# Optimization experiments

Hardware: AMD Instinct MI355X
Metric: run time of the kernel (lower is better)

Reference implementation:

```python
import jax, jax.numpy as jnp
import numpy as np

V, D, J = 1024, 1024, 1024  # num_outputs, predictor_dim, joiner_dim
B, U = 64, 512
NULL_INDEX = 0


def setup_inputs() -> dict:
    key = jax.random.key(0)
    ks = jax.random.split(key, 9)
    s = 0.02
    return {
        "y": jax.random.randint(ks[0], (B, U), 0, V, dtype=jnp.int64) if jax.config.jax_enable_x64 else jax.random.randint(ks[0], (B, U), 0, V, dtype=jnp.int32),
        "embed": jax.random.normal(ks[1], (V, D), jnp.float32) * s,
        "weight_ih": jax.random.normal(ks[2], (3 * D, D), jnp.float32) * s,
        "bias_ih": jax.random.normal(ks[3], (3 * D,), jnp.float32) * s,
        "weight_hh": jax.random.normal(ks[4], (3 * D, D), jnp.float32) * s,
        "bias_hh": jax.random.normal(ks[5], (3 * D,), jnp.float32) * s,
        "linear_w": jax.random.normal(ks[6], (J, D), jnp.float32) * s,
        "linear_b": jax.random.normal(ks[7], (J,), jnp.float32) * s,
        "initial_state": jax.random.normal(ks[8], (D,), jnp.float32),
    }


def reference(y, embed, weight_ih, bias_ih, weight_hh, bias_hh, linear_w, linear_b, initial_state):
    b, u_len = y.shape
    d = initial_state.shape[0]
    # Decoder input sequence: start symbol (NULL_INDEX=0) then the labels -> length U+1
    tokens = jnp.concatenate([jnp.full((b, 1), NULL_INDEX, dtype=y.dtype), y], axis=1)  # [B, U+1]
    x = embed[tokens]  # [B, U+1, D]
    # Precompute input-side gate pre-activations for all steps (batched GEMM)
    gx = jnp.einsum("bud,gd->bug", x, weight_ih) + bias_ih  # [B, U+1, 3D]
    h0 = jnp.broadcast_to(initial_state, (b, d))

    def step(h, gx_t):
        # PyTorch GRUCell: gates ordered (r, z, n)
        gh = h @ weight_hh.T + bias_hh  # [B, 3D]
        r = jax.nn.sigmoid(gx_t[:, :d] + gh[:, :d])
        z = jax.nn.sigmoid(gx_t[:, d:2 * d] + gh[:, d:2 * d])
        n = jnp.tanh(gx_t[:, 2 * d:] + r * gh[:, 2 * d:])
        h_new = (1.0 - z) * n + z * h
        return h_new, h_new

    _, hs = jax.lax.scan(step, h0, jnp.swapaxes(gx, 0, 1))  # hs: [U+1, B, D]
    out = jnp.einsum("ubd,jd->buj", hs, linear_w) + linear_b  # [B, U+1, J]
    return out
```

## Files before the change

### kernel.cpp

```cpp
#include <hip/hip_runtime.h>
#include <hip/hip_bf16.h>

typedef float f32x4 __attribute__((ext_vector_type(4)));
typedef short s16x8 __attribute__((ext_vector_type(8)));
typedef int   i32x4 __attribute__((ext_vector_type(4)));
typedef _Float16 h16x8 __attribute__((ext_vector_type(8)));

#define NV 1024
#define ND 1024
#define NJ 1024
#define NB 64
#define NU 512
#define NT 513
#define G3 3072
#define SLOT 65536
#define NWG 64

static __device__ __forceinline__ unsigned short f2h(float f) {
  union { _Float16 h; unsigned short u; } x; x.h = (_Float16)f;
  return x.u;
}

static __device__ __forceinline__ void unswizzle(long e, int& r, int& k) {
  long blk = e >> 9; int l = (int)((e >> 3) & 63); int j = (int)(e & 7);
  r = (int)(blk >> 5) * 16 + (l & 15);
  k = ((int)(blk & 31)) * 32 + ((l >> 4) << 3) + j;
}

__global__ void predictor_prep(const float* __restrict__ whh, const float* __restrict__ wih,
                               const float* __restrict__ em, const float* __restrict__ lw,
                               const float* __restrict__ bih, const float* __restrict__ bhh,
                               const float* __restrict__ init,
                               unsigned short* __restrict__ wh_sw, unsigned short* __restrict__ wi_sw,
                               unsigned short* __restrict__ em_sw, unsigned short* __restrict__ lw_sw,
                               float* __restrict__ bias_sum, unsigned short* __restrict__ hs,
                               unsigned int* __restrict__ flags) {
  long e = (long)blockIdx.x * 256 + threadIdx.x;
  const long nbig = 3145728, nsm = 1048576;
  if (e < nbig) { int r, k; unswizzle(e, r, k); wh_sw[e] = f2h(whh[(long)r * 1024 + k]); return; }
  e -= nbig;
  if (e < nbig) { int r, k; unswizzle(e, r, k); wi_sw[e] = f2h(wih[(long)r * 1024 + k]); return; }
  e -= nbig;
  if (e < nsm) { int r, k; unswizzle(e, r, k); em_sw[e] = f2h(em[(long)r * 1024 + k]); return; }
  e -= nsm;
  if (e < nsm) { int r, k; unswizzle(e, r, k); lw_sw[e] = f2h(lw[(long)r * 1024 + k]); return; }
  e -= nsm;
  if (e < 65536) { int r, k; unswizzle(e, r, k); hs[e] = f2h(init[k]); return; }
  e -= 65536;
  if (e < 3072) { bias_sum[e] = bih[e] + bhh[e]; return; }
  e -= 3072;
  if (e < 128) flags[e] = 0u;
}

__global__ __launch_bounds__(256) void predictor_gemm(
    const unsigned short* __restrict__ A, long a_chunk_stride,
    const unsigned short* __restrict__ Bw,
    const float* __restrict__ bias, float* __restrict__ out,
    int rowmul_i, int rowmul_c, int out_stride) {
  const int nt = blockIdx.x, chunk = blockIdx.y;
  const int tid = threadIdx.x, lane = tid & 63, wave = tid >> 6;
  const unsigned short* Ab = A + (long)chunk * a_chunk_stride + wave * 16384 + lane * 8;
  const unsigned short* Bb = Bw + (long)nt * 65536 + lane * 8;
  f32x4 a0 = {0,0,0,0}, a1 = {0,0,0,0}, a2 = {0,0,0,0}, a3 = {0,0,0,0};
#pragma unroll 4
  for (int kc = 0; kc < 32; ++kc) {
    h16x8 av = __builtin_bit_cast(h16x8, *(const s16x8*)(Ab + kc * 512));
    h16x8 w0 = __builtin_bit_cast(h16x8, *(const s16x8*)(Bb + kc * 512));
    h16x8 w1 = __builtin_bit_cast(h16x8, *(const s16x8*)(Bb + 16384 + kc * 512));
    h16x8 w2 = __builtin_bit_cast(h16x8, *(const s16x8*)(Bb + 32768 + kc * 512));
    h16x8 w3 = __builtin_bit_cast(h16x8, *(const s16x8*)(Bb + 49152 + kc * 512));
    a0 = __builtin_amdgcn_mfma_f32_16x16x32_f16(av, w0, a0, 0, 0, 0);
    a1 = __builtin_amdgcn_mfma_f32_16x16x32_f16(av, w1, a1, 0, 0, 0);
    a2 = __builtin_amdgcn_mfma_f32_16x16x32_f16(av, w2, a2, 0, 0, 0);
    a3 = __builtin_amdgcn_mfma_f32_16x16x32_f16(av, w3, a3, 0, 0, 0);
  }
  const int q = lane >> 4, nl = lane & 15, colbase = nt << 6;
#pragma unroll
  for (int j = 0; j < 4; ++j) {
    int il = (wave << 4) + (q << 2) + j;
    long row = (long)il * rowmul_i + (long)chunk * rowmul_c;
    float* orow = out + row * out_stride + colbase;
    orow[nl]      = a0[j] + bias[colbase + nl];
    orow[16 + nl] = a1[j] + bias[colbase + 16 + nl];
    orow[32 + nl] = a2[j] + bias[colbase + 32 + nl];
    orow[48 + nl] = a3[j] + bias[colbase + 48 + nl];
  }
}

#define PINSTAGE(CNT, B)                                                        \
  asm volatile("s_waitcnt vmcnt(" #CNT ")"                                      \
    : "+v"(hf[(B)*8+0]), "+v"(hf[(B)*8+1]), "+v"(hf[(B)*8+2]), "+v"(hf[(B)*8+3]), \
      "+v"(hf[(B)*8+4]), "+v"(hf[(B)*8+5]), "+v"(hf[(B)*8+6]), "+v"(hf[(B)*8+7]) :: "memory")

__global__ __launch_bounds__(256, 1) void predictor_rnn(
    const unsigned short* __restrict__ wh_sw, const float* __restrict__ gtab,
    const int* __restrict__ y, const float* __restrict__ init,
    unsigned short* __restrict__ hs, unsigned short* __restrict__ flags) {
  __shared__ float buf[4][3][4][64][4];
  __shared__ unsigned short tbuf[1024];
  const int wg = blockIdx.x, tid = threadIdx.x, lane = tid & 63, w = tid >> 6;
  const int q = lane >> 4, dloc = lane & 15, dg = (wg << 4) + dloc;

  h16x8 wrf[8], wzf[8], wnf[8];
#pragma unroll
  for (int i = 0; i < 8; ++i) {
    int kc = (w << 3) + i;
    wrf[i] = __builtin_bit_cast(h16x8, *(const s16x8*)(wh_sw + ((long)(      wg) << 14) + kc * 512 + lane * 8));
    wzf[i] = __builtin_bit_cast(h16x8, *(const s16x8*)(wh_sw + ((long)( 64 + wg) << 14) + kc * 512 + lane * 8));
    wnf[i] = __builtin_bit_cast(h16x8, *(const s16x8*)(wh_sw + ((long)(128 + wg) << 14) + kc * 512 + lane * 8));
  }
  float hreg[4];
#pragma unroll
  for (int j = 0; j < 4; ++j) hreg[j] = init[dg];

  const unsigned short* fpoll = flags + (w << 6) + lane;
  unsigned short* fpub = flags + ((wg >> 4) << 6) + ((wg & 15) << 2) + w;

  for (int t = 1; t <= NT; ++t) {
    float gr[4], gz[4], gn[4];
#pragma unroll
    for (int j = 0; j < 4; ++j) {
      int b = (w << 4) + (q << 2) + j;
      int tok = (t == 1) ? 0 : y[b * NU + (t - 2)];
      const float* g = gtab + (long)tok * G3 + dg;
      asm volatile("global_load_dword %0, %1, off" : "=v"(gr[j]) : "v"(g) : "memory");
      asm volatile("global_load_dword %0, %1, off" : "=v"(gz[j]) : "v"(g + 1024) : "memory");
      asm volatile("global_load_dword %0, %1, off" : "=v"(gn[j]) : "v"(g + 2048) : "memory");
    }

    if (t > 1) {
      const unsigned int tm1 = (unsigned)(t - 1);
      for (;;) {
        unsigned int v;
        asm volatile("global_load_ushort %0, %1, off sc1" : "=v"(v) : "v"(fpoll) : "memory");
        asm volatile("s_waitcnt vmcnt(0)" : "+v"(v) :: "memory");
        if (__all((int)(v >= tm1))) break;
        __builtin_amdgcn_s_sleep(1);
      }
    }
    asm volatile("s_waitcnt vmcnt(0)"
      : "+v"(gr[0]), "+v"(gr[1]), "+v"(gr[2]), "+v"(gr[3]),
        "+v"(gz[0]), "+v"(gz[1]), "+v"(gz[2]), "+v"(gz[3]),
        "+v"(gn[0]), "+v"(gn[1]), "+v"(gn[2]), "+v"(gn[3]) :: "memory");

    const unsigned short* hprev = hs + (long)(t - 1) * SLOT;
    unsigned short* hcur = hs + (long)t * SLOT;

    i32x4 hf[32];
#pragma unroll
    for (int bg = 0; bg < 4; ++bg)
#pragma unroll
      for (int i = 0; i < 8; ++i) {
        const unsigned short* a = hprev + bg * 16384 + ((w << 3) + i) * 512 + lane * 8;
        asm volatile("global_load_dwordx4 %0, %1, off sc1" : "=v"(hf[bg * 8 + i]) : "v"(a) : "memory");
      }
    f32x4 aR[4], aZ[4], aN[4];
#pragma unroll
    for (int bg = 0; bg < 4; ++bg) { aR[bg] = (f32x4){0,0,0,0}; aZ[bg] = (f32x4){0,0,0,0}; aN[bg] = (f32x4){0,0,0,0}; }
    {
      PINSTAGE(24, 0);
#pragma unroll
      for (int i = 0; i < 8; ++i) { h16x8 a = __builtin_bit_cast(h16x8, hf[0 * 8 + i]);
        aR[0] = __builtin_amdgcn_mfma_f32_16x16x32_f16(a, wrf[i], aR[0], 0, 0, 0);
        aZ[0] = __builtin_amdgcn_mfma_f32_16x16x32_f16(a, wzf[i], aZ[0], 0, 0, 0);
        aN[0] = __builtin_amdgcn_mfma_f32_16x16x32_f16(a, wnf[i], aN[0], 0, 0, 0); }
      PINSTAGE(16, 1);
#pragma unroll
      for (int i = 0; i < 8; ++i) { h16x8 a = __builtin_bit_cast(h16x8, hf[1 * 8 + i]);
        aR[1] = __builtin_amdgcn_mfma_f32_16x16x32_f16(a, wrf[i], aR[1], 0, 0, 0);
        aZ[1] = __builtin_amdgcn_mfma_f32_16x16x32_f16(a, wzf[i], aZ[1], 0, 0, 0);
        aN[1] = __builtin_amdgcn_mfma_f32_16x16x32_f16(a, wnf[i], aN[1], 0, 0, 0); }
      PINSTAGE(8, 2);
#pragma unroll
      for (int i = 0; i < 8; ++i) { h16x8 a = __builtin_bit_cast(h16x8, hf[2 * 8 + i]);
        aR[2] = __builtin_amdgcn_mfma_f32_16x16x32_f16(a, wrf[i], aR[2], 0, 0, 0);
        aZ[2] = __builtin_amdgcn_mfma_f32_16x16x32_f16(a, wzf[i], aZ[2], 0, 0, 0);
        aN[2] = __builtin_amdgcn_mfma_f32_16x16x32_f16(a, wnf[i], aN[2], 0, 0, 0); }
      PINSTAGE(0, 3);
#pragma unroll
      for (int i = 0; i < 8; ++i) { h16x8 a = __builtin_bit_cast(h16x8, hf[3 * 8 + i]);
        aR[3] = __builtin_amdgcn_mfma_f32_16x16x32_f16(a, wrf[i], aR[3], 0, 0, 0);
        aZ[3] = __builtin_amdgcn_mfma_f32_16x16x32_f16(a, wzf[i], aZ[3], 0, 0, 0);
        aN[3] = __builtin_amdgcn_mfma_f32_16x16x32_f16(a, wnf[i], aN[3], 0, 0, 0); }
    }

#pragma unroll
    for (int b2 = 0; b2 < 4; ++b2)
      if (b2 != w) {
        *(f32x4*)&buf[w][0][b2][lane][0] = aR[b2];
        *(f32x4*)&buf[w][1][b2][lane][0] = aZ[b2];
        *(f32x4*)&buf[w][2][b2][lane][0] = aN[b2];
      }
    __syncthreads();
    f32x4 sR = aR[w], sZ = aZ[w], sN = aN[w];
#pragma unroll
    for (int v = 0; v < 4; ++v)
      if (v != w) {
        sR += *(const f32x4*)&buf[v][0][w][lane][0];
        sZ += *(const f32x4*)&buf[v][1][w][lane][0];
        sN += *(const f32x4*)&buf[v][2][w][lane][0];
      }
    __syncthreads();

#pragma unroll
    for (int j = 0; j < 4; ++j) {
      float r = 1.f / (1.f + __expf(-(gr[j] + sR[j])));
      float z = 1.f / (1.f + __expf(-(gz[j] + sZ[j])));
      float np = gn[j] + r * sN[j];
      float e2 = __expf(-2.f * fabsf(np));
      float tn = (1.f - e2) / (1.f + e2);
      tn = np < 0.f ? -tn : tn;
      float hnew = (1.f - z) * tn + z * hreg[j];
      hreg[j] = hnew;
      tbuf[(w << 8) + ((((q << 2) + j) | ((dloc >> 3) << 4)) << 3) + (dloc & 7)] = f2h(hnew);
    }
    asm volatile("s_waitcnt lgkmcnt(0)" ::: "memory");

    {
      unsigned long long pv = *(const unsigned long long*)(tbuf + (w << 8) + lane * 4);
      unsigned short* gp = hcur + ((long)(w * 32 + (wg >> 1)) << 9) + ((wg & 1) << 8) + lane * 4;
      asm volatile("global_store_dwordx2 %0, %1, off sc1" :: "v"(gp), "v"(pv) : "memory");
      asm volatile("s_waitcnt vmcnt(0)" ::: "memory");
      if (lane == 0)
        asm volatile("global_store_short %0, %1, off sc1" :: "v"(fpub), "v"((unsigned)t) : "memory");
    }
  }
}

extern "C" void kernel_launch(void* const* d_in, const int* in_sizes, int n_in,
                              void* d_out, int out_size, void* d_ws, size_t ws_size,
                              hipStream_t stream) {
  const int*   y    = (const int*)d_in[0];
  const float* em   = (const float*)d_in[1];
  const float* wih  = (const float*)d_in[2];
  const float* bih  = (const float*)d_in[3];
  const float* whh  = (const float*)d_in[4];
  const float* bhh  = (const float*)d_in[5];
  const float* lw   = (const float*)d_in[6];
  const float* lb   = (const float*)d_in[7];
  const float* init = (const float*)d_in[8];
  float* out = (float*)d_out;

  char* ws = (char*)d_ws;
  size_t off = 0;
  auto alloc = [&](size_t n) { void* p = ws + off; off += (n + 255) & ~(size_t)255; return p; };
  unsigned short* wh_sw   = (unsigned short*)alloc(6291456);
  unsigned short* wi_sw   = (unsigned short*)alloc(6291456);
  unsigned short* em_sw   = (unsigned short*)alloc(2097152);
  unsigned short* lw_sw   = (unsigned short*)alloc(2097152);
  float*          gtab    = (float*)alloc(12582912);
  float*          bias_sum= (float*)alloc(12288);
  unsigned int*   flags   = (unsigned int*)alloc(512);
  unsigned short* hs      = (unsigned short*)alloc(67371008UL);
  (void)ws_size; (void)in_sizes; (void)n_in; (void)out_size;

  predictor_prep<<<dim3(33037), dim3(256), 0, stream>>>(
      whh, wih, em, lw, bih, bhh, init, wh_sw, wi_sw, em_sw, lw_sw, bias_sum, hs, flags);
  predictor_gemm<<<dim3(48, 16), dim3(256), 0, stream>>>(
      em_sw, 65536L, wi_sw, bias_sum, gtab, 1, 64, 3072);
  predictor_rnn<<<dim3(NWG), dim3(256), 0, stream>>>(
      wh_sw, gtab, y, init, hs, (unsigned short*)flags);
  predictor_gemm<<<dim3(16, 513), dim3(256), 0, stream>>>(
      hs + 65536, 65536L, lw_sw, lb, out, 513, 1, 1024);
}
```

Measured before the change: 3.143 ms.

## Split GRU recurrence by batch per wave with LDS-resident weights, drop cross-wave reduction

```diff
diff --git a/kernel.cpp b/kernel.cpp
--- a/kernel.cpp
+++ b/kernel.cpp
@@ -96,25 +96,28 @@
     const unsigned short* __restrict__ wh_sw, const float* __restrict__ gtab,
     const int* __restrict__ y, const float* __restrict__ init,
     unsigned short* __restrict__ hs, unsigned short* __restrict__ flags) {
-  __shared__ float buf[4][3][4][64][4];
+  __shared__ unsigned short wlds[49152];
   __shared__ unsigned short tbuf[1024];
   const int wg = blockIdx.x, tid = threadIdx.x, lane = tid & 63, w = tid >> 6;
   const int q = lane >> 4, dloc = lane & 15, dg = (wg << 4) + dloc;
 
-  h16x8 wrf[8], wzf[8], wnf[8];
-#pragma unroll
-  for (int i = 0; i < 8; ++i) {
-    int kc = (w << 3) + i;
-    wrf[i] = __builtin_bit_cast(h16x8, *(const s16x8*)(wh_sw + ((long)(      wg) << 14) + kc * 512 + lane * 8));
-    wzf[i] = __builtin_bit_cast(h16x8, *(const s16x8*)(wh_sw + ((long)( 64 + wg) << 14) + kc * 512 + lane * 8));
-    wnf[i] = __builtin_bit_cast(h16x8, *(const s16x8*)(wh_sw + ((long)(128 + wg) << 14) + kc * 512 + lane * 8));
-  }
+  for (int g = 0; g < 3; ++g) {
+    const unsigned short* src = wh_sw + ((long)(g * 64 + wg) << 14);
+#pragma unroll
+    for (int i = 0; i < 8; ++i) {
+      int c = i * 256 + tid;
+      *(s16x8*)&wlds[g * 16384 + c * 8] = *(const s16x8*)&src[c * 8];
+    }
+  }
+  __syncthreads();
+
   float hreg[4];
 #pragma unroll
   for (int j = 0; j < 4; ++j) hreg[j] = init[dg];
 
   const unsigned short* fpoll = flags + (w << 6) + lane;
-  unsigned short* fpub = flags + ((wg >> 4) << 6) + ((wg & 15) << 2) + w;
+  unsigned short* fpub = flags + (w << 6) + wg;
+  const s16x8* wbase = (const s16x8*)wlds + lane;
 
   for (int t = 1; t <= NT; ++t) {
     float gr[4], gz[4], gn[4];
@@ -143,70 +146,60 @@
         "+v"(gz[0]), "+v"(gz[1]), "+v"(gz[2]), "+v"(gz[3]),
         "+v"(gn[0]), "+v"(gn[1]), "+v"(gn[2]), "+v"(gn[3]) :: "memory");
 
-    const unsigned short* hprev = hs + (long)(t - 1) * SLOT;
+    const unsigned short* hprev = hs + (long)(t - 1) * SLOT + (w << 14);
     unsigned short* hcur = hs + (long)t * SLOT;
 
     i32x4 hf[32];
 #pragma unroll
-    for (int bg = 0; bg < 4; ++bg)
-#pragma unroll
-      for (int i = 0; i < 8; ++i) {
-        const unsigned short* a = hprev + bg * 16384 + ((w << 3) + i) * 512 + lane * 8;
-        asm volatile("global_load_dwordx4 %0, %1, off sc1" : "=v"(hf[bg * 8 + i]) : "v"(a) : "memory");
-      }
-    f32x4 aR[4], aZ[4], aN[4];
-#pragma unroll
-    for (int bg = 0; bg < 4; ++bg) { aR[bg] = (f32x4){0,0,0,0}; aZ[bg] = (f32x4){0,0,0,0}; aN[bg] = (f32x4){0,0,0,0}; }
+    for (int i = 0; i < 32; ++i) {
+      const unsigned short* a = hprev + i * 512 + lane * 8;
+      asm volatile("global_load_dwordx4 %0, %1, off sc1" : "=v"(hf[i]) : "v"(a) : "memory");
+    }
+    f32x4 aR = {0,0,0,0}, aZ = {0,0,0,0}, aN = {0,0,0,0};
     {
       PINSTAGE(24, 0);
 #pragma unroll
-      for (int i = 0; i < 8; ++i) { h16x8 a = __builtin_bit_cast(h16x8, hf[0 * 8 + i]);
-        aR[0] = __builtin_amdgcn_mfma_f32_16x16x32_f16(a, wrf[i], aR[0], 0, 0, 0);
-        aZ[0] = __builtin_amdgcn_mfma_f32_16x16x32_f16(a, wzf[i], aZ[0], 0, 0, 0);
-        aN[0] = __builtin_amdgcn_mfma_f32_16x16x32_f16(a, wnf[i], aN[0], 0, 0, 0); }
+      for (int i = 0; i < 8; ++i) { int kc = i; h16x8 a = __builtin_bit_cast(h16x8, hf[kc]);
+        h16x8 wr = __builtin_bit_cast(h16x8, wbase[kc * 64]);
+        h16x8 wz = __builtin_bit_cast(h16x8, wbase[2048 + kc * 64]);
+        h16x8 wn = __builtin_bit_cast(h16x8, wbase[4096 + kc * 64]);
+        aR = __builtin_amdgcn_mfma_f32_16x16x32_f16(a, wr, aR, 0, 0, 0);
+        aZ = __builtin_amdgcn_mfma_f32_16x16x32_f16(a, wz, aZ, 0, 0, 0);
+        aN = __builtin_amdgcn_mfma_f32_16x16x32_f16(a, wn, aN, 0, 0, 0); }
       PINSTAGE(16, 1);
 #pragma unroll
-      for (int i = 0; i < 8; ++i) { h16x8 a = __builtin_bit_cast(h16x8, hf[1 * 8 + i]);
-        aR[1] = __builtin_amdgcn_mfma_f32_16x16x32_f16(a, wrf[i], aR[1], 0, 0, 0);
-        aZ[1] = __builtin_amdgcn_mfma_f32_16x16x32_f16(a, wzf[i], aZ[1], 0, 0, 0);
-        aN[1] = __builtin_amdgcn_mfma_f32_16x16x32_f16(a, wnf[i], aN[1], 0, 0, 0); }
+      for (int i = 0; i < 8; ++i) { int kc = 8 + i; h16x8 a = __builtin_bit_cast(h16x8, hf[kc]);
+        h16x8 wr = __builtin_bit_cast(h16x8, wbase[kc * 64]);
+        h16x8 wz = __builtin_bit_cast(h16x8, wbase[2048 + kc * 64]);
+        h16x8 wn = __builtin_bit_cast(h16x8, wbase[4096 + kc * 64]);
+        aR = __builtin_amdgcn_mfma_f32_16x16x32_f16(a, wr, aR, 0, 0, 0);
+        aZ = __builtin_amdgcn_mfma_f32_16x16x32_f16(a, wz, aZ, 0, 0, 0);
+        aN = __builtin_amdgcn_mfma_f32_16x16x32_f16(a, wn, aN, 0, 0, 0); }
       PINSTAGE(8, 2);
 #pragma unroll
-      for (int i = 0; i < 8; ++i) { h16x8 a = __builtin_bit_cast(h16x8, hf[2 * 8 + i]);
-        aR[2] = __builtin_amdgcn_mfma_f32_16x16x32_f16(a, wrf[i], aR[2], 0, 0, 0);
-        aZ[2] = __builtin_amdgcn_mfma_f32_16x16x32_f16(a, wzf[i], aZ[2], 0, 0, 0);
-        aN[2] = __builtin_amdgcn_mfma_f32_16x16x32_f16(a, wnf[i], aN[2], 0, 0, 0); }
+      for (int i = 0; i < 8; ++i) { int kc = 16 + i; h16x8 a = __builtin_bit_cast(h16x8, hf[kc]);
+        h16x8 wr = __builtin_bit_cast(h16x8, wbase[kc * 64]);
+        h16x8 wz = __builtin_bit_cast(h16x8, wbase[2048 + kc * 64]);
+        h16x8 wn = __builtin_bit_cast(h16x8, wbase[4096 + kc * 64]);
+        aR = __builtin_amdgcn_mfma_f32_16x16x32_f16(a, wr, aR, 0, 0, 0);
+        aZ = __builtin_amdgcn_mfma_f32_16x16x32_f16(a, wz, aZ, 0, 0, 0);
+        aN = __builtin_amdgcn_mfma_f32_16x16x32_f16(a, wn, aN, 0, 0, 0); }
       PINSTAGE(0, 3);
 #pragma unroll
-      for (int i = 0; i < 8; ++i) { h16x8 a = __builtin_bit_cast(h16x8, hf[3 * 8 + i]);
-        aR[3] = __builtin_amdgcn_mfma_f32_16x16x32_f16(a, wrf[i], aR[3], 0, 0, 0);
-        aZ[3] = __builtin_amdgcn_mfma_f32_16x16x32_f16(a, wzf[i], aZ[3], 0, 0, 0);
-        aN[3] = __builtin_amdgcn_mfma_f32_16x16x32_f16(a, wnf[i], aN[3], 0, 0, 0); }
-    }
-
-#pragma unroll
-    for (int b2 = 0; b2 < 4; ++b2)
-      if (b2 != w) {
-        *(f32x4*)&buf[w][0][b2][lane][0] = aR[b2];
-        *(f32x4*)&buf[w][1][b2][lane][0] = aZ[b2];
-        *(f32x4*)&buf[w][2][b2][lane][0] = aN[b2];
-      }
-    __syncthreads();
-    f32x4 sR = aR[w], sZ = aZ[w], sN = aN[w];
-#pragma unroll
-    for (int v = 0; v < 4; ++v)
-      if (v != w) {
-        sR += *(const f32x4*)&buf[v][0][w][lane][0];
-        sZ += *(const f32x4*)&buf[v][1][w][lane][0];
-        sN += *(const f32x4*)&buf[v][2][w][lane][0];
-      }
-    __syncthreads();
+      for (int i = 0; i < 8; ++i) { int kc = 24 + i; h16x8 a = __builtin_bit_cast(h16x8, hf[kc]);
+        h16x8 wr = __builtin_bit_cast(h16x8, wbase[kc * 64]);
+        h16x8 wz = __builtin_bit_cast(h16x8, wbase[2048 + kc * 64]);
+        h16x8 wn = __builtin_bit_cast(h16x8, wbase[4096 + kc * 64]);
+        aR = __builtin_amdgcn_mfma_f32_16x16x32_f16(a, wr, aR, 0, 0, 0);
+        aZ = __builtin_amdgcn_mfma_f32_16x16x32_f16(a, wz, aZ, 0, 0, 0);
+        aN = __builtin_amdgcn_mfma_f32_16x16x32_f16(a, wn, aN, 0, 0, 0); }
+    }
 
 #pragma unroll
     for (int j = 0; j < 4; ++j) {
-      float r = 1.f / (1.f + __expf(-(gr[j] + sR[j])));
-      float z = 1.f / (1.f + __expf(-(gz[j] + sZ[j])));
-      float np = gn[j] + r * sN[j];
+      float r = 1.f / (1.f + __expf(-(gr[j] + aR[j])));
+      float z = 1.f / (1.f + __expf(-(gz[j] + aZ[j])));
+      float np = gn[j] + r * aN[j];
       float e2 = __expf(-2.f * fabsf(np));
       float tn = (1.f - e2) / (1.f + e2);
       tn = np < 0.f ? -tn : tn;
```

Result: faster. 2.876 ms (-8.5%).
